# Performance work log

Measured on AMD Instinct MI355X. Metric: run time of the kernel, lower is better.

Reference implementation:

```python
import jax, jax.numpy as jnp
import numpy as np

M_CODES = 512
D_EMB = 128
COMMITMENT = 0.25
DECAY = 0.999
EPS = 1e-05


def setup_inputs() -> dict:
    key = jax.random.key(0)
    k1, k2, k3 = jax.random.split(key, 3)
    B, T = 32, 2048
    init_bound = 1.0 / M_CODES
    embedding = jax.random.uniform(k2, (M_CODES, D_EMB), jnp.float32, -init_bound, init_bound)
    return {
        'x': jax.random.normal(k1, (B, T, D_EMB), jnp.float32),
        'x_mask': jnp.ones((B, 1, T), jnp.float32),
        'embedding': embedding,
        'ema_count': jnp.zeros((M_CODES,), jnp.float32),
        'ema_weight': embedding,  # clone of embedding at init
    }


def reference(x, x_mask, embedding, ema_count, ema_weight):
    mask = jnp.transpose(x_mask, (0, 2, 1))  # [B, T, 1]
    xm = x * mask                            # masked input (named `x` in torch code)
    M, D = embedding.shape
    x_flat = jax.lax.stop_gradient(xm).reshape(-1, D)  # [N, D], N = B*T
    distances = (jnp.sum(embedding ** 2, axis=1)[None, :]
                 + jnp.sum(x_flat ** 2, axis=1, keepdims=True)
                 - 2.0 * (x_flat @ embedding.T))  # [N, M]
    indices = jnp.argmin(distances.astype(jnp.float32), axis=-1)  # [N]
    quantized = embedding[indices].reshape(xm.shape)  # gather + view_as(x)
    # --- EMA codebook update (training branch) ---
    # sum of one-hot encodings over tokens == per-code counts
    counts = jax.ops.segment_sum(jnp.ones_like(x_flat[:, 0]), indices, num_segments=M)
    new_count = DECAY * ema_count + (1.0 - DECAY) * counts
    n = jnp.sum(new_count)
    new_count = (new_count + EPS) / (n + M * EPS) * n
    # encodings.T @ x_flat == scatter-add of token features per code
    dw = jax.ops.segment_sum(x_flat, indices, num_segments=M)  # [M, D]
    new_weight = DECAY * ema_weight + (1.0 - DECAY) * dw
    new_embedding = new_weight / new_count[:, None]
    # --- commitment loss (quantized detached) ---
    e_latent_loss = jnp.sum((xm * mask - jax.lax.stop_gradient(quantized) * mask) ** 2) / (jnp.sum(mask) * x.shape[-1])
    loss = COMMITMENT * e_latent_loss
    # straight-through estimator
    q_st = (xm + jax.lax.stop_gradient(quantized - xm)) * mask
    return (q_st, loss, new_embedding, new_count, new_weight)
```

## Files before the change

### kernel.cpp

```cpp
#include <hip/hip_runtime.h>

#define M_CODES 512
#define D_EMB 128
#define D4 32
#define MARGIN 5e-5f
#define SCHUNK 1024
#define ADSTRIDE 513

typedef short bf16x8 __attribute__((ext_vector_type(8)));
typedef float f32x4 __attribute__((ext_vector_type(4)));

__device__ __forceinline__ unsigned short f2bf(float f) {
    unsigned u = __float_as_uint(f);
    u += 0x7fffu + ((u >> 16) & 1u);
    return (unsigned short)(u >> 16);
}
__device__ __forceinline__ float bf2f(unsigned short h) {
    return __uint_as_float(((unsigned)h) << 16);
}

__device__ __forceinline__ float np_pairwise_sumsq128(const float* __restrict__ a,
                                                      float scale) {
    float r[8];
#pragma unroll
    for (int j = 0; j < 8; ++j) {
        float v = __fmul_rn(a[j], scale);
        r[j] = __fmul_rn(v, v);
    }
    for (int i = 8; i < 128; i += 8) {
#pragma unroll
        for (int j = 0; j < 8; ++j) {
            float v = __fmul_rn(a[i + j], scale);
            r[j] = __fadd_rn(r[j], __fmul_rn(v, v));
        }
    }
    return __fadd_rn(__fadd_rn(__fadd_rn(r[0], r[1]), __fadd_rn(r[2], r[3])),
                     __fadd_rn(__fadd_rn(r[4], r[5]), __fadd_rn(r[6], r[7])));
}

__global__ __launch_bounds__(256) void kSZ(const float* __restrict__ emb,
                                           float* __restrict__ sumE,
                                           float* __restrict__ embT,
                                           unsigned short* __restrict__ ebh,
                                           unsigned short* __restrict__ ebl,
                                           float* __restrict__ accc,
                                           int* __restrict__ flagCnt) {
    int tid = threadIdx.x, wid = tid >> 6, lane = tid & 63;
    int m = blockIdx.x * 4 + wid;
    int gi = blockIdx.x * 256 + tid;
    if (gi < M_CODES) accc[gi] = 0.f;
    if (gi == 0) *flagCnt = 0;
    const float* er = emb + (size_t)m * D_EMB;
    float r = 0.f;
    if (lane < 8) {
        float v = __fmul_rn(er[lane], 1.0f);
        r = __fmul_rn(v, v);
        for (int i = 1; i < 16; ++i) {
            float w = __fmul_rn(er[8 * i + lane], 1.0f);
            r = __fadd_rn(r, __fmul_rn(w, w));
        }
    }
    float s1 = __fadd_rn(r, __shfl_xor(r, 1, 64));
    float s2 = __fadd_rn(s1, __shfl_xor(s1, 2, 64));
    float s3 = __fadd_rn(s2, __shfl_xor(s2, 4, 64));
    if (lane == 0) sumE[m] = s3;
#pragma unroll
    for (int dd = lane; dd < D_EMB; dd += 64) {
        float e = er[dd];
        embT[dd * M_CODES + m] = e;
        unsigned short hh = f2bf(e);
        ebh[(size_t)m * D_EMB + dd] = hh;
        ebl[(size_t)m * D_EMB + dd] = f2bf(e - bf2f(hh));
    }
}

__global__ __launch_bounds__(256) void kA(const float* __restrict__ x,
                                          const float* __restrict__ xmask,
                                          const unsigned short* __restrict__ ebh,
                                          const unsigned short* __restrict__ ebl,
                                          const float* __restrict__ sumE,
                                          int* __restrict__ idx_out,
                                          int* __restrict__ flagCnt,
                                          int* __restrict__ flagList,
                                          float* __restrict__ lossW,
                                          float* __restrict__ maskW, int N) {
    __shared__ unsigned short hb[2][4096];
    __shared__ unsigned short lb[2][4096];
    __shared__ float xnS[4][32], mkS[4][32];
    int tid = threadIdx.x;
    int wid = tid >> 6, lane = tid & 63;
    int m = lane & 15, kg = lane >> 4;
    int tok0 = blockIdx.x * 128 + wid * 32;

    bf16x8 ah0[4], al0[4], ah1[4], al1[4];
    float xn0 = 0.f, xn1 = 0.f;
    float mk0 = xmask[tok0 + m], mk1 = xmask[tok0 + 16 + m];
#pragma unroll
    for (int ks = 0; ks < 4; ++ks) {
        const float4* p0 = reinterpret_cast<const float4*>(
            x + (size_t)(tok0 + m) * D_EMB + ks * 32 + kg * 8);
        const float4* p1 = reinterpret_cast<const float4*>(
            x + (size_t)(tok0 + 16 + m) * D_EMB + ks * 32 + kg * 8);
        float4 a0 = p0[0], a1 = p0[1], c0 = p1[0], c1 = p1[1];
        float e0[8] = {a0.x, a0.y, a0.z, a0.w, a1.x, a1.y, a1.z, a1.w};
        float e1[8] = {c0.x, c0.y, c0.z, c0.w, c1.x, c1.y, c1.z, c1.w};
        bf16x8 h0, l0, h1, l1;
#pragma unroll
        for (int j = 0; j < 8; ++j) {
            float v0 = e0[j] * mk0;
            xn0 = fmaf(v0, v0, xn0);
            unsigned short hh0 = f2bf(v0);
            h0[j] = (short)hh0;
            l0[j] = (short)f2bf(v0 - bf2f(hh0));
            float v1 = e1[j] * mk1;
            xn1 = fmaf(v1, v1, xn1);
            unsigned short hh1 = f2bf(v1);
            h1[j] = (short)hh1;
            l1[j] = (short)f2bf(v1 - bf2f(hh1));
        }
        ah0[ks] = h0; al0[ks] = l0; ah1[ks] = h1; al1[ks] = l1;
    }
    xn0 += __shfl_xor(xn0, 16, 64);
    xn0 += __shfl_xor(xn0, 32, 64);
    xn1 += __shfl_xor(xn1, 16, 64);
    xn1 += __shfl_xor(xn1, 32, 64);
    if (kg == 0) {
        xnS[wid][m] = xn0; mkS[wid][m] = mk0;
        xnS[wid][16 + m] = xn1; mkS[wid][16 + m] = mk1;
    }

    float b1[2][4], b2[2][4];
    int bi[2][4];
#pragma unroll
    for (int tt = 0; tt < 2; ++tt)
#pragma unroll
        for (int r = 0; r < 4; ++r) {
            b1[tt][r] = 3.4e38f; b2[tt][r] = 3.4e38f; bi[tt][r] = 0x7fffffff;
        }

    int mo = tid >> 4, sl = tid & 15;
    int dstIdx = mo * 128 + (sl >> 3) * 64 + ((sl & 7) ^ (mo & 7)) * 8;
    float4 sh0, sv0, sh1, sv1;
#define LOADREGS(t)                                                            \
    {                                                                          \
        sh0 = *reinterpret_cast<const float4*>(                                \
            ebh + (size_t)((t) * 32 + mo) * D_EMB + sl * 8);                   \
        sv0 = *reinterpret_cast<const float4*>(                                \
            ebl + (size_t)((t) * 32 + mo) * D_EMB + sl * 8);                   \
        sh1 = *reinterpret_cast<const float4*>(                                \
            ebh + (size_t)((t) * 32 + 16 + mo) * D_EMB + sl * 8);              \
        sv1 = *reinterpret_cast<const float4*>(                                \
            ebl + (size_t)((t) * 32 + 16 + mo) * D_EMB + sl * 8);              \
    }
#define WRITEB(b)                                                              \
    {                                                                          \
        *reinterpret_cast<float4*>(&hb[b][dstIdx]) = sh0;                      \
        *reinterpret_cast<float4*>(&lb[b][dstIdx]) = sv0;                      \
        *reinterpret_cast<float4*>(&hb[b][2048 + dstIdx]) = sh1;               \
        *reinterpret_cast<float4*>(&lb[b][2048 + dstIdx]) = sv1;               \
    }

    LOADREGS(0);
    WRITEB(0);
    __syncthreads();
    for (int t = 0; t < 16; ++t) {
        int cur = t & 1;
        if (t < 15) LOADREGS(t + 1);
#pragma unroll
        for (int sub = 0; sub < 2; ++sub) {
            bf16x8 bh[4], bl[4];
#pragma unroll
            for (int ks = 0; ks < 4; ++ks) {
                int off = sub * 2048 + m * 128 + (ks >> 1) * 64 +
                          ((((ks & 1) * 4 + kg)) ^ (m & 7)) * 8;
                bh[ks] = *reinterpret_cast<const bf16x8*>(&hb[cur][off]);
                bl[ks] = *reinterpret_cast<const bf16x8*>(&lb[cur][off]);
            }
            f32x4 accA0 = {0.f, 0.f, 0.f, 0.f}, accB0 = {0.f, 0.f, 0.f, 0.f};
            f32x4 accA1 = {0.f, 0.f, 0.f, 0.f}, accB1 = {0.f, 0.f, 0.f, 0.f};
#pragma unroll
            for (int ks = 0; ks < 2; ++ks) {
                accA0 = __builtin_amdgcn_mfma_f32_16x16x32_bf16(ah0[ks], bh[ks], accA0, 0, 0, 0);
                accA0 = __builtin_amdgcn_mfma_f32_16x16x32_bf16(al0[ks], bh[ks], accA0, 0, 0, 0);
                accA0 = __builtin_amdgcn_mfma_f32_16x16x32_bf16(ah0[ks], bl[ks], accA0, 0, 0, 0);
                accA1 = __builtin_amdgcn_mfma_f32_16x16x32_bf16(ah1[ks], bh[ks], accA1, 0, 0, 0);
                accA1 = __builtin_amdgcn_mfma_f32_16x16x32_bf16(al1[ks], bh[ks], accA1, 0, 0, 0);
                accA1 = __builtin_amdgcn_mfma_f32_16x16x32_bf16(ah1[ks], bl[ks], accA1, 0, 0, 0);
            }
#pragma unroll
            for (int ks = 2; ks < 4; ++ks) {
                accB0 = __builtin_amdgcn_mfma_f32_16x16x32_bf16(ah0[ks], bh[ks], accB0, 0, 0, 0);
                accB0 = __builtin_amdgcn_mfma_f32_16x16x32_bf16(al0[ks], bh[ks], accB0, 0, 0, 0);
                accB0 = __builtin_amdgcn_mfma_f32_16x16x32_bf16(ah0[ks], bl[ks], accB0, 0, 0, 0);
                accB1 = __builtin_amdgcn_mfma_f32_16x16x32_bf16(ah1[ks], bh[ks], accB1, 0, 0, 0);
                accB1 = __builtin_amdgcn_mfma_f32_16x16x32_bf16(al1[ks], bh[ks], accB1, 0, 0, 0);
                accB1 = __builtin_amdgcn_mfma_f32_16x16x32_bf16(ah1[ks], bl[ks], accB1, 0, 0, 0);
            }
            int c = t * 32 + sub * 16 + m;
            float sE = sumE[c];
#pragma unroll
            for (int r = 0; r < 4; ++r) {
                float s0 = fmaf(-2.f, accA0[r] + accB0[r], sE);
                if (s0 < b1[0][r]) { b2[0][r] = b1[0][r]; b1[0][r] = s0; bi[0][r] = c; }
                else if (s0 < b2[0][r]) b2[0][r] = s0;
                float s1 = fmaf(-2.f, accA1[r] + accB1[r], sE);
                if (s1 < b1[1][r]) { b2[1][r] = b1[1][r]; b1[1][r] = s1; bi[1][r] = c; }
                else if (s1 < b2[1][r]) b2[1][r] = s1;
            }
        }
        if (t < 15) WRITEB(cur ^ 1);
        __syncthreads();
    }
#undef LOADREGS
#undef WRITEB
#pragma unroll
    for (int off = 1; off <= 8; off <<= 1) {
#pragma unroll
        for (int tt = 0; tt < 2; ++tt)
#pragma unroll
            for (int r = 0; r < 4; ++r) {
                float o1 = __shfl_xor(b1[tt][r], off, 64);
                float o2 = __shfl_xor(b2[tt][r], off, 64);
                int oi = __shfl_xor(bi[tt][r], off, 64);
                if (o1 < b1[tt][r] || (o1 == b1[tt][r] && oi < bi[tt][r])) {
                    b2[tt][r] = fminf(b1[tt][r], o2); b1[tt][r] = o1; bi[tt][r] = oi;
                } else {
                    b2[tt][r] = fminf(b2[tt][r], o1);
                }
            }
    }
    float liS = 0.f, mkT = 0.f;
#pragma unroll
    for (int tt = 0; tt < 2; ++tt)
#pragma unroll
        for (int r = 0; r < 4; ++r) {
            int row = kg * 4 + r;
            float mkr = mkS[wid][tt * 16 + row], xnr = xnS[wid][tt * 16 + row];
            liS += mkr * mkr * (xnr + b1[tt][r]);
            mkT += mkr;
            if (m == 0) {
                int tokr = tok0 + tt * 16 + row;
                idx_out[tokr] = bi[tt][r];
                if (b2[tt][r] - b1[tt][r] < MARGIN) {
                    int pp = atomicAdd(flagCnt, 1);
                    flagList[pp] = tokr;
                }
            }
        }
    liS += __shfl_xor(liS, 16, 64);
    liS += __shfl_xor(liS, 32, 64);
    mkT += __shfl_xor(mkT, 16, 64);
    mkT += __shfl_xor(mkT, 32, 64);
    if (lane == 0) {
        int grp = blockIdx.x * 4 + wid;
        lossW[grp] = liS;
        maskW[grp] = mkT;
    }
}

__global__ __launch_bounds__(256) void kF(const float* __restrict__ x,
                                          const float* __restrict__ xmask,
                                          const float* __restrict__ embT,
                                          const float* __restrict__ sumE,
                                          const int* __restrict__ flagCnt,
                                          const int* __restrict__ flagList,
                                          int* __restrict__ idx_out) {
    int wave = (blockIdx.x * 256 + threadIdx.x) >> 6;
    int lane = threadIdx.x & 63;
    int nW = gridDim.x * 4;
    int cnt = *flagCnt;
    for (int j = wave; j < cnt; j += nW) {
        int t = flagList[j];
        float mk = xmask[t];
        const float* xr = x + (size_t)t * D_EMB;
        float sx = np_pairwise_sumsq128(xr, mk);
        float acc[8];
#pragma unroll
        for (int cb = 0; cb < 8; ++cb) acc[cb] = 0.f;
        for (int i = 0; i < D_EMB; ++i) {
            float xi = __fmul_rn(xr[i], mk);
#pragma unroll
            for (int cb = 0; cb < 8; ++cb)
                acc[cb] = __fmaf_rn(xi, embT[i * M_CODES + cb * 64 + lane], acc[cb]);
        }
        float best = 3.4e38f;
        int bq = 0x7fffffff;
#pragma unroll
        for (int cb = 0; cb < 8; ++cb) {
            int c = cb * 64 + lane;
            float d = __fsub_rn(__fadd_rn(sumE[c], sx), __fmul_rn(2.f, acc[cb]));
            if (d < best || (d == best && c < bq)) { best = d; bq = c; }
        }
#pragma unroll
        for (int off = 32; off > 0; off >>= 1) {
            float s2 = __shfl_xor(best, off, 64);
            int i2 = __shfl_xor(bq, off, 64);
            if (s2 < best || (s2 == best && i2 < bq)) { best = s2; bq = i2; }
        }
        if (lane == 0) idx_out[t] = bq;
    }
}

__global__ __launch_bounds__(1024) void kScat(const float* __restrict__ x,
                                              const float* __restrict__ emb,
                                              const float* __restrict__ xmask,
                                              const int* __restrict__ idx,
                                              float* __restrict__ q_st,
                                              float* __restrict__ partialD,
                                              float* __restrict__ accc,
                                              int N, int nch) {
    __shared__ float accD[32 * ADSTRIDE];
    __shared__ int idxL[SCHUNK];
    __shared__ float mkL[SCHUNK];
    __shared__ float accC[M_CODES];
    int bid = blockIdx.x;
    int q = bid / nch, ch = bid - q * nch;
    int tid = threadIdx.x;
    for (int i = tid; i < 32 * ADSTRIDE; i += 1024) accD[i] = 0.f;
    if (q == 0)
        for (int i = tid; i < M_CODES; i += 1024) accC[i] = 0.f;
    int base = ch * SCHUNK;
    idxL[tid] = idx[base + tid];
    mkL[tid] = xmask[base + tid];
    __syncthreads();
    if (q == 0) atomicAdd(&accC[idxL[tid]], 1.f);
    int tl = tid >> 3, dl = tid & 7;
    for (int it = 0; it < SCHUNK / 128; ++it) {
        int t = it * 128 + tl;
        int id = idxL[t];
        float mk = mkL[t];
        size_t fo = (size_t)(base + t) * D4 + q * 8 + dl;
        float4 xv = reinterpret_cast<const float4*>(x)[fo];
        float4 ev = reinterpret_cast<const float4*>(emb)[(size_t)id * D4 + q * 8 + dl];
        float4 o;
        o.x = ev.x * mk; o.y = ev.y * mk; o.z = ev.z * mk; o.w = ev.w * mk;
        reinterpret_cast<float4*>(q_st)[fo] = o;
        int d0 = dl * 4;
        atomicAdd(&accD[(d0 + 0) * ADSTRIDE + id], xv.x * mk);
        atomicAdd(&accD[(d0 + 1) * ADSTRIDE + id], xv.y * mk);
        atomicAdd(&accD[(d0 + 2) * ADSTRIDE + id], xv.z * mk);
        atomicAdd(&accD[(d0 + 3) * ADSTRIDE + id], xv.w * mk);
    }
    __syncthreads();
    float* pD = partialD + (size_t)bid * (32 * M_CODES);
    for (int i = tid; i < 32 * M_CODES; i += 1024) {
        int dd = i >> 9, c = i & 511;
        pD[i] = accD[dd * ADSTRIDE + c];
    }
    if (q == 0)
        for (int i = tid; i < M_CODES; i += 1024) atomicAdd(&accc[i], accC[i]);
}

__global__ __launch_bounds__(256) void kWD2(const float* __restrict__ partialD,
                                            const float* __restrict__ ema_w,
                                            const float* __restrict__ counts,
                                            const float* __restrict__ ema_count,
                                            const float* __restrict__ lossP,
                                            const float* __restrict__ maskP,
                                            float* __restrict__ new_w,
                                            float* __restrict__ new_emb,
                                            float* __restrict__ new_cnt,
                                            float* __restrict__ loss_out,
                                            int nch, int nP) {
    __shared__ float red[256];
    int tid = threadIdx.x;
    float part = 0.999f * ema_count[tid] + 0.001f * counts[tid];
    part += 0.999f * ema_count[tid + 256] + 0.001f * counts[tid + 256];
    red[tid] = part;
    __syncthreads();
#pragma unroll
    for (int s = 128; s > 0; s >>= 1) {
        if (tid < s) red[tid] += red[tid + s];
        __syncthreads();
    }
    float nsum = red[0];
    __syncthreads();

    int i = blockIdx.x * 256 + tid;
    int c = i & 511;
    int d = i >> 9;
    int q = d >> 5, dd = d & 31;
    float raw = 0.999f * ema_count[c] + 0.001f * counts[c];
    float norm = (raw + 1e-5f) / (nsum + (float)M_CODES * 1e-5f) * nsum;
    float s = 0.f;
    for (int ch = 0; ch < nch; ++ch)
        s += partialD[(size_t)(q * nch + ch) * (32 * M_CODES) + dd * M_CODES + c];
    size_t o = (size_t)c * D_EMB + d;
    float w = 0.999f * ema_w[o] + 0.001f * s;
    new_w[o] = w;
    new_emb[o] = w / norm;
    if (d == 0) new_cnt[c] = norm;

    if (blockIdx.x == 0) {
        float lp = 0.f, mp = 0.f;
        for (int j = tid; j < nP; j += 256) { lp += lossP[j]; mp += maskP[j]; }
        red[tid] = lp;
        __syncthreads();
#pragma unroll
        for (int ss = 128; ss > 0; ss >>= 1) {
            if (tid < ss) red[tid] += red[tid + ss];
            __syncthreads();
        }
        float S = red[0];
        __syncthreads();
        red[tid] = mp;
        __syncthreads();
#pragma unroll
        for (int ss = 128; ss > 0; ss >>= 1) {
            if (tid < ss) red[tid] += red[tid + ss];
            __syncthreads();
        }
        if (tid == 0) loss_out[0] = 0.25f * S / (red[0] * (float)D_EMB);
    }
}

extern "C" void kernel_launch(void* const* d_in, const int* in_sizes, int n_in,
                              void* d_out, int out_size, void* d_ws, size_t ws_size,
                              hipStream_t stream) {
    const float* x = (const float*)d_in[0];
    const float* xmask = (const float*)d_in[1];
    const float* emb = (const float*)d_in[2];
    const float* ema_count = (const float*)d_in[3];
    const float* ema_weight = (const float*)d_in[4];
    int N = in_sizes[0] / D_EMB;

    float* out = (float*)d_out;
    float* q_st = out;
    float* loss = out + (size_t)N * D_EMB;
    float* new_emb = loss + 1;
    float* new_cnt = new_emb + M_CODES * D_EMB;
    float* new_w = new_cnt + M_CODES;

    int nGrp = N / 32;
    int nch = (N + SCHUNK - 1) / SCHUNK;
    float* fws = (float*)d_ws;
    int* idx = (int*)fws;
    float* counts = fws + N;
    float* norm = counts + M_CODES;
    float* lossP = norm + M_CODES;
    float* maskP = lossP + nGrp;
    float* sumE = maskP + nGrp;
    int* flagCnt = (int*)(sumE + M_CODES);
    int* flagList = flagCnt + 4;
    float* embT = (float*)(flagList + N);
    unsigned short* ebh = (unsigned short*)(embT + M_CODES * D_EMB);
    unsigned short* ebl = ebh + M_CODES * D_EMB;
    float* partialD = (float*)(ebl + M_CODES * D_EMB);

    hipLaunchKernelGGL(kSZ, dim3(128), dim3(256), 0, stream,
                       emb, sumE, embT, ebh, ebl, counts, flagCnt);
    hipLaunchKernelGGL(kA, dim3(N / 128), dim3(256), 0, stream, x, xmask, ebh,
                       ebl, sumE, idx, flagCnt, flagList, lossP, maskP, N);
    hipLaunchKernelGGL(kF, dim3(1024), dim3(256), 0, stream, x, xmask, embT, sumE,
                       flagCnt, flagList, idx);
    hipLaunchKernelGGL(kScat, dim3(4 * nch), dim3(1024), 0, stream, x, emb,
                       xmask, idx, q_st, partialD, counts, N, nch);
    hipLaunchKernelGGL(kWD2, dim3(M_CODES * D_EMB / 256), dim3(256), 0, stream,
                       partialD, ema_weight, counts, ema_count, lossP, maskP,
                       new_w, new_emb, new_cnt, loss, nch, nGrp);
}
```

Before: 135.2 us.

## Replace shared-atomic scatter with counting-sort bucketing and per-code gather aggregation

Replaces the shared-memory atomic scatter-add, with its per-chunk partial buffers and cross-chunk reduction, by a counting sort. The new pipeline builds a histogram of code indices, takes a prefix sum, and buckets token ids by code. One block per code then gathers its tokens to sum features and write q_st, with no atomics on features. The cost is three extra small launches, including a single-block prefix kernel. Token-to-block work is very imbalanced, since one block handles all tokens of a popular code, and bucket order is nondeterministic, so the float summation order varies between runs.

```diff
diff --git a/kernel.cpp b/kernel.cpp
--- a/kernel.cpp
+++ b/kernel.cpp
@@ -5,7 +5,6 @@
 #define D4 32
 #define MARGIN 5e-5f
 #define SCHUNK 1024
-#define ADSTRIDE 513
 
 typedef short bf16x8 __attribute__((ext_vector_type(8)));
 typedef float f32x4 __attribute__((ext_vector_type(4)));
@@ -43,12 +42,12 @@
                                            float* __restrict__ embT,
                                            unsigned short* __restrict__ ebh,
                                            unsigned short* __restrict__ ebl,
-                                           float* __restrict__ accc,
+                                           int* __restrict__ gcnt,
                                            int* __restrict__ flagCnt) {
     int tid = threadIdx.x, wid = tid >> 6, lane = tid & 63;
     int m = blockIdx.x * 4 + wid;
     int gi = blockIdx.x * 256 + tid;
-    if (gi < M_CODES) accc[gi] = 0.f;
+    if (gi < M_CODES) gcnt[gi] = 0;
     if (gi == 0) *flagCnt = 0;
     const float* er = emb + (size_t)m * D_EMB;
     float r = 0.f;
@@ -301,116 +300,137 @@
     }
 }
 
-__global__ __launch_bounds__(1024) void kScat(const float* __restrict__ x,
-                                              const float* __restrict__ emb,
-                                              const float* __restrict__ xmask,
-                                              const int* __restrict__ idx,
-                                              float* __restrict__ q_st,
-                                              float* __restrict__ partialD,
-                                              float* __restrict__ accc,
-                                              int N, int nch) {
-    __shared__ float accD[32 * ADSTRIDE];
-    __shared__ int idxL[SCHUNK];
-    __shared__ float mkL[SCHUNK];
-    __shared__ float accC[M_CODES];
-    int bid = blockIdx.x;
-    int q = bid / nch, ch = bid - q * nch;
+__global__ __launch_bounds__(1024) void kHist(const int* __restrict__ idx,
+                                              int* __restrict__ gcnt) {
+    __shared__ int h[M_CODES];
     int tid = threadIdx.x;
-    for (int i = tid; i < 32 * ADSTRIDE; i += 1024) accD[i] = 0.f;
-    if (q == 0)
-        for (int i = tid; i < M_CODES; i += 1024) accC[i] = 0.f;
-    int base = ch * SCHUNK;
-    idxL[tid] = idx[base + tid];
-    mkL[tid] = xmask[base + tid];
-    __syncthreads();
-    if (q == 0) atomicAdd(&accC[idxL[tid]], 1.f);
-    int tl = tid >> 3, dl = tid & 7;
-    for (int it = 0; it < SCHUNK / 128; ++it) {
-        int t = it * 128 + tl;
-        int id = idxL[t];
-        float mk = mkL[t];
-        size_t fo = (size_t)(base + t) * D4 + q * 8 + dl;
-        float4 xv = reinterpret_cast<const float4*>(x)[fo];
-        float4 ev = reinterpret_cast<const float4*>(emb)[(size_t)id * D4 + q * 8 + dl];
-        float4 o;
-        o.x = ev.x * mk; o.y = ev.y * mk; o.z = ev.z * mk; o.w = ev.w * mk;
-        reinterpret_cast<float4*>(q_st)[fo] = o;
-        int d0 = dl * 4;
-        atomicAdd(&accD[(d0 + 0) * ADSTRIDE + id], xv.x * mk);
-        atomicAdd(&accD[(d0 + 1) * ADSTRIDE + id], xv.y * mk);
-        atomicAdd(&accD[(d0 + 2) * ADSTRIDE + id], xv.z * mk);
-        atomicAdd(&accD[(d0 + 3) * ADSTRIDE + id], xv.w * mk);
-    }
-    __syncthreads();
-    float* pD = partialD + (size_t)bid * (32 * M_CODES);
-    for (int i = tid; i < 32 * M_CODES; i += 1024) {
-        int dd = i >> 9, c = i & 511;
-        pD[i] = accD[dd * ADSTRIDE + c];
-    }
-    if (q == 0)
-        for (int i = tid; i < M_CODES; i += 1024) atomicAdd(&accc[i], accC[i]);
-}
-
-__global__ __launch_bounds__(256) void kWD2(const float* __restrict__ partialD,
-                                            const float* __restrict__ ema_w,
-                                            const float* __restrict__ counts,
+    if (tid < M_CODES) h[tid] = 0;
+    __syncthreads();
+    atomicAdd(&h[idx[blockIdx.x * 1024 + tid]], 1);
+    __syncthreads();
+    if (tid < M_CODES && h[tid] > 0) atomicAdd(&gcnt[tid], h[tid]);
+}
+
+__global__ __launch_bounds__(512) void kPfx(const int* __restrict__ gcnt,
                                             const float* __restrict__ ema_count,
+                                            int* __restrict__ offs,
+                                            int* __restrict__ cursor,
+                                            float* __restrict__ normv,
+                                            float* __restrict__ new_cnt,
                                             const float* __restrict__ lossP,
                                             const float* __restrict__ maskP,
+                                            float* __restrict__ loss_out, int nP) {
+    __shared__ int sc[M_CODES];
+    __shared__ float red[M_CODES];
+    int tid = threadIdx.x;
+    int c = gcnt[tid];
+    sc[tid] = c;
+    __syncthreads();
+    for (int off = 1; off < M_CODES; off <<= 1) {
+        int v = (tid >= off) ? sc[tid - off] : 0;
+        __syncthreads();
+        sc[tid] += v;
+        __syncthreads();
+    }
+    int excl = sc[tid] - c;
+    offs[tid] = excl;
+    cursor[tid] = excl;
+    float raw = 0.999f * ema_count[tid] + 0.001f * (float)c;
+    red[tid] = raw;
+    __syncthreads();
+#pragma unroll
+    for (int s = 256; s > 0; s >>= 1) {
+        if (tid < s) red[tid] += red[tid + s];
+        __syncthreads();
+    }
+    float nsum = red[0];
+    __syncthreads();
+    float nrm = (raw + 1e-5f) / (nsum + (float)M_CODES * 1e-5f) * nsum;
+    normv[tid] = nrm;
+    new_cnt[tid] = nrm;
+    float lp = 0.f, mp = 0.f;
+    for (int j = tid; j < nP; j += 512) { lp += lossP[j]; mp += maskP[j]; }
+    red[tid] = lp;
+    __syncthreads();
+#pragma unroll
+    for (int s = 256; s > 0; s >>= 1) {
+        if (tid < s) red[tid] += red[tid + s];
+        __syncthreads();
+    }
+    float S = red[0];
+    __syncthreads();
+    red[tid] = mp;
+    __syncthreads();
+#pragma unroll
+    for (int s = 256; s > 0; s >>= 1) {
+        if (tid < s) red[tid] += red[tid + s];
+        __syncthreads();
+    }
+    if (tid == 0) loss_out[0] = 0.25f * S / (red[0] * (float)D_EMB);
+}
+
+__global__ __launch_bounds__(1024) void kBucket(const int* __restrict__ idx,
+                                                int* __restrict__ cursor,
+                                                int* __restrict__ bucket) {
+    __shared__ int lh[M_CODES];
+    __shared__ int gb[M_CODES];
+    int tid = threadIdx.x;
+    if (tid < M_CODES) lh[tid] = 0;
+    __syncthreads();
+    int t = blockIdx.x * 1024 + tid;
+    int c = idx[t];
+    int r = atomicAdd(&lh[c], 1);
+    __syncthreads();
+    if (tid < M_CODES && lh[tid] > 0) gb[tid] = atomicAdd(&cursor[tid], lh[tid]);
+    __syncthreads();
+    bucket[gb[c] + r] = t;
+}
+
+__global__ __launch_bounds__(256) void kAgg(const float* __restrict__ x,
+                                            const float* __restrict__ xmask,
+                                            const float* __restrict__ emb,
+                                            const float* __restrict__ ema_w,
+                                            const int* __restrict__ bucket,
+                                            const int* __restrict__ offs,
+                                            const int* __restrict__ gcnt,
+                                            const float* __restrict__ normv,
+                                            float* __restrict__ q_st,
                                             float* __restrict__ new_w,
-                                            float* __restrict__ new_emb,
-                                            float* __restrict__ new_cnt,
-                                            float* __restrict__ loss_out,
-                                            int nch, int nP) {
-    __shared__ float red[256];
+                                            float* __restrict__ new_emb) {
+    __shared__ int tokL[256];
+    __shared__ float mkL[256];
+    __shared__ float half1[D_EMB];
+    int c = blockIdx.x;
     int tid = threadIdx.x;
-    float part = 0.999f * ema_count[tid] + 0.001f * counts[tid];
-    part += 0.999f * ema_count[tid + 256] + 0.001f * counts[tid + 256];
-    red[tid] = part;
-    __syncthreads();
-#pragma unroll
-    for (int s = 128; s > 0; s >>= 1) {
-        if (tid < s) red[tid] += red[tid + s];
-        __syncthreads();
-    }
-    float nsum = red[0];
-    __syncthreads();
-
-    int i = blockIdx.x * 256 + tid;
-    int c = i & 511;
-    int d = i >> 9;
-    int q = d >> 5, dd = d & 31;
-    float raw = 0.999f * ema_count[c] + 0.001f * counts[c];
-    float norm = (raw + 1e-5f) / (nsum + (float)M_CODES * 1e-5f) * nsum;
-    float s = 0.f;
-    for (int ch = 0; ch < nch; ++ch)
-        s += partialD[(size_t)(q * nch + ch) * (32 * M_CODES) + dd * M_CODES + c];
-    size_t o = (size_t)c * D_EMB + d;
-    float w = 0.999f * ema_w[o] + 0.001f * s;
-    new_w[o] = w;
-    new_emb[o] = w / norm;
-    if (d == 0) new_cnt[c] = norm;
-
-    if (blockIdx.x == 0) {
-        float lp = 0.f, mp = 0.f;
-        for (int j = tid; j < nP; j += 256) { lp += lossP[j]; mp += maskP[j]; }
-        red[tid] = lp;
-        __syncthreads();
-#pragma unroll
-        for (int ss = 128; ss > 0; ss >>= 1) {
-            if (tid < ss) red[tid] += red[tid + ss];
-            __syncthreads();
-        }
-        float S = red[0];
-        __syncthreads();
-        red[tid] = mp;
-        __syncthreads();
-#pragma unroll
-        for (int ss = 128; ss > 0; ss >>= 1) {
-            if (tid < ss) red[tid] += red[tid + ss];
-            __syncthreads();
-        }
-        if (tid == 0) loss_out[0] = 0.25f * S / (red[0] * (float)D_EMB);
+    int d = tid & 127, par = tid >> 7;
+    int off = offs[c], cnt = gcnt[c];
+    float e = emb[(size_t)c * D_EMB + d];
+    float dw = 0.f;
+    for (int base = 0; base < cnt; base += 256) {
+        int n = cnt - base;
+        if (n > 256) n = 256;
+        if (tid < n) {
+            int t = bucket[off + base + tid];
+            tokL[tid] = t;
+            mkL[tid] = xmask[t];
+        }
+        __syncthreads();
+        for (int i = par; i < n; i += 2) {
+            int t = tokL[i];
+            float mk = mkL[i];
+            dw = fmaf(x[(size_t)t * D_EMB + d], mk, dw);
+            q_st[(size_t)t * D_EMB + d] = e * mk;
+        }
+        __syncthreads();
+    }
+    if (par == 1) half1[d] = dw;
+    __syncthreads();
+    if (par == 0) {
+        float s = dw + half1[d];
+        size_t o = (size_t)c * D_EMB + d;
+        float w = 0.999f * ema_w[o] + 0.001f * s;
+        new_w[o] = w;
+        new_emb[o] = w / normv[c];
     }
 }
 
@@ -432,30 +452,35 @@
     float* new_w = new_cnt + M_CODES;
 
     int nGrp = N / 32;
-    int nch = (N + SCHUNK - 1) / SCHUNK;
+    int nch = N / 1024;
     float* fws = (float*)d_ws;
     int* idx = (int*)fws;
-    float* counts = fws + N;
-    float* norm = counts + M_CODES;
-    float* lossP = norm + M_CODES;
+    int* gcnt = idx + N;
+    int* offs = gcnt + M_CODES;
+    int* cursor = offs + M_CODES;
+    float* normv = (float*)(cursor + M_CODES);
+    float* lossP = normv + M_CODES;
     float* maskP = lossP + nGrp;
     float* sumE = maskP + nGrp;
     int* flagCnt = (int*)(sumE + M_CODES);
     int* flagList = flagCnt + 4;
-    float* embT = (float*)(flagList + N);
+    int* bucket = flagList + N;
+    float* embT = (float*)(bucket + N);
     unsigned short* ebh = (unsigned short*)(embT + M_CODES * D_EMB);
     unsigned short* ebl = ebh + M_CODES * D_EMB;
-    float* partialD = (float*)(ebl + M_CODES * D_EMB);
 
     hipLaunchKernelGGL(kSZ, dim3(128), dim3(256), 0, stream,
-                       emb, sumE, embT, ebh, ebl, counts, flagCnt);
+                       emb, sumE, embT, ebh, ebl, gcnt, flagCnt);
     hipLaunchKernelGGL(kA, dim3(N / 128), dim3(256), 0, stream, x, xmask, ebh,
                        ebl, sumE, idx, flagCnt, flagList, lossP, maskP, N);
     hipLaunchKernelGGL(kF, dim3(1024), dim3(256), 0, stream, x, xmask, embT, sumE,
                        flagCnt, flagList, idx);
-    hipLaunchKernelGGL(kScat, dim3(4 * nch), dim3(1024), 0, stream, x, emb,
-                       xmask, idx, q_st, partialD, counts, N, nch);
-    hipLaunchKernelGGL(kWD2, dim3(M_CODES * D_EMB / 256), dim3(256), 0, stream,
-                       partialD, ema_weight, counts, ema_count, lossP, maskP,
-                       new_w, new_emb, new_cnt, loss, nch, nGrp);
-}
+    hipLaunchKernelGGL(kHist, dim3(nch), dim3(1024), 0, stream, idx, gcnt);
+    hipLaunchKernelGGL(kPfx, dim3(1), dim3(512), 0, stream, gcnt, ema_count,
+                       offs, cursor, normv, new_cnt, lossP, maskP, loss, nGrp);
+    hipLaunchKernelGGL(kBucket, dim3(nch), dim3(1024), 0, stream, idx, cursor,
+                       bucket);
+    hipLaunchKernelGGL(kAgg, dim3(M_CODES), dim3(256), 0, stream, x, xmask, emb,
+                       ema_weight, bucket, offs, gcnt, normv, q_st, new_w,
+                       new_emb);
+}
```

Measured after the change: 122.1 us. 1.11x faster.
